# Kernel optimization log

Measured on AMD Instinct MI355X. Metric: run time of the kernel, lower is better.

The kernel has to match this reference:

```python
import jax, jax.numpy as jnp
import numpy as np

N, D, R, T, E = 4096, 1024, 92, 32, 8192
SCALE = float(np.sqrt(2.0 / 7.0))  # matches torch.rand(...) * sqrt(2/7)


def setup_inputs() -> dict:
    key = jax.random.key(0)
    ks = jax.random.split(key, 7)
    x = jax.random.normal(ks[0], (N, D), dtype=jnp.float32)
    edge_tok = jax.random.randint(ks[1], (E,), 0, N)
    edge_rel = jax.random.randint(ks[2], (E,), 0, R)
    W_stack = jax.random.uniform(ks[3], (R, D, D), dtype=jnp.float32) * SCALE  # depWeights
    B_stack = jnp.ones((R, D), dtype=jnp.float32)                              # depBias
    W_self = jax.random.uniform(ks[4], (D, D), dtype=jnp.float32) * SCALE      # self.weight
    b_self = jnp.ones((D,), dtype=jnp.float32)                                 # self.bias
    W_tag = jax.random.normal(ks[5], (D, T), dtype=jnp.float32) * 0.02         # hidden2tag
    b_tag = jnp.zeros((T,), dtype=jnp.float32)
    return {"x": x, "W_self": W_self, "b_self": b_self, "W_stack": W_stack,
            "B_stack": B_stack, "W_tag": W_tag, "b_tag": b_tag,
            "edge_tok": edge_tok, "edge_rel": edge_rel}


def reference(x, W_self, b_self, W_stack, B_stack, W_tag, b_tag, edge_tok, edge_rel):
    n, r = x.shape[0], W_stack.shape[0]
    # C[i, r] = number of dependency edges of token i with relation r
    C = jnp.zeros((n, r), dtype=x.dtype).at[edge_tok, edge_rel].add(jnp.asarray(1.0, x.dtype))
    self_out = x @ W_self + b_self  # [N, D]
    # accum_i = self_out_i + sum_{dep in deps(i)} (x_i @ W_dep + b_dep)
    #         = self_out_i + sum_r C[i, r] * (x_i @ W_r) + (C @ B_stack)_i
    def body(acc, wc):
        Wr, Cr = wc  # Wr: [D, D], Cr: [N]
        return acc + Cr[:, None] * (x @ Wr), None
    dep_out, _ = jax.lax.scan(body, jnp.zeros_like(self_out), (W_stack, C.T))
    h = jax.nn.relu(self_out + dep_out + C @ B_stack)  # [N, D]
    tag_scores = jax.nn.log_softmax(h @ W_tag + b_tag, axis=1)  # [N, T]
    return tag_scores, h
```

## Files before the change

kernel.cpp:

```cpp
#include <hip/hip_runtime.h>
#include <hip/hip_bf16.h>
#include <math.h>

#define N_TOK 4096
#define D_DIM 1024
#define R_REL 92
#define T_TAG 32
#define E_EDGE 8192
#define SELF_R 127
#define GRID_ITEMS 192


typedef short bf16x8 __attribute__((ext_vector_type(8)));
typedef float f32x4 __attribute__((ext_vector_type(4)));

union Pk8 { uint4 q; unsigned short s[8]; };
union Pk4 { uint2 d; unsigned short s[4]; };

__device__ __forceinline__ unsigned short f2bf(float f) {
    union { __hip_bfloat16 b; unsigned short u; } c;
    c.b = __float2bfloat16(f);
    return c.u;
}
__device__ __forceinline__ float bf2f(unsigned short u) {
    return __uint_as_float(((unsigned)u) << 16);
}
__device__ __forceinline__ void gload_lds16(const void* g, void* l) {
    __builtin_amdgcn_global_load_lds(
        (const __attribute__((address_space(1))) unsigned int*)g,
        (__attribute__((address_space(3))) unsigned int*)l, 16, 0, 0);
}

__global__ __launch_bounds__(1024) void k_prep(const int* __restrict__ rel,
                                               const int* __restrict__ tokv,
                                               const float* __restrict__ x,
                                               int* __restrict__ ws,
                                               unsigned short* __restrict__ xb) {
    int t = threadIdx.x;
    if (blockIdx.x > 0) {
        size_t base = ((size_t)(blockIdx.x - 1) * 1024 + t) * 8;
        float4 v0 = *(const float4*)(x + base);
        float4 v1 = *(const float4*)(x + base + 4);
        Pk8 u;
        u.s[0] = f2bf(v0.x); u.s[1] = f2bf(v0.y);
        u.s[2] = f2bf(v0.z); u.s[3] = f2bf(v0.w);
        u.s[4] = f2bf(v1.x); u.s[5] = f2bf(v1.y);
        u.s[6] = f2bf(v1.z); u.s[7] = f2bf(v1.w);
        *(uint4*)(xb + base) = u.q;
        return;
    }
    __shared__ int cnt[128], offL[128], cur[128];
    __shared__ int sh[128];
    __shared__ int wsum[16];
    __shared__ int tcnt[4096], toff[4096];
    int lane = t & 63, wid = t >> 6;
    if (t < 128) { cnt[t] = 0; cur[t] = 0; }
    #pragma unroll
    for (int i = 0; i < 4; ++i) tcnt[i * 1024 + t] = 0;
    __syncthreads();
    int er[8], et[8];
    #pragma unroll
    for (int i = 0; i < 8; ++i) {
        er[i] = rel[i * 1024 + t];
        et[i] = tokv[i * 1024 + t];
        atomicAdd(&cnt[er[i]], 1);
        atomicAdd(&tcnt[et[i]], 1);
    }
    __syncthreads();
    int c = (t < 128) ? cnt[t] : 0;
    int v = c;
    if (t < 128) sh[t] = v;
    __syncthreads();
    for (int st = 1; st < 128; st <<= 1) {
        int add = (t >= st && t < 128) ? sh[t - st] : 0;
        __syncthreads();
        if (t < 128) { v += add; sh[t] = v; }
        __syncthreads();
    }
    if (t < 128) { offL[t] = v - c; ws[256 + t] = v - c; ws[t] = c; }
    int ch = (t < R_REL) ? ((c + 127) >> 7) : 0;
    int v2 = ch;
    if (t < 128) sh[t] = v2;
    __syncthreads();
    for (int st = 1; st < 128; st <<= 1) {
        int add = (t >= st && t < 128) ? sh[t - st] : 0;
        __syncthreads();
        if (t < 128) { v2 += add; sh[t] = v2; }
        __syncthreads();
    }
    if (t < 32) ws[512 + t] = (SELF_R << 16) | t;
    if (t < R_REL) {
        int excl = v2 - ch;
        for (int j = 0; j < ch; ++j)
            ws[512 + 32 + excl + j] = (t << 16) | j;
    }
    if (t == 127) ws[384] = 32 + v2;
    int s0 = tcnt[4 * t + 0], s1 = tcnt[4 * t + 1];
    int s2 = tcnt[4 * t + 2], s3 = tcnt[4 * t + 3];
    int sum4 = s0 + s1 + s2 + s3;
    int vv = sum4;
    #pragma unroll
    for (int d = 1; d < 64; d <<= 1) {
        int n = __shfl_up(vv, d);
        if (lane >= d) vv += n;
    }
    if (lane == 63) wsum[wid] = vv;
    __syncthreads();
    if (wid == 0) {
        int wv = (lane < 16) ? wsum[lane] : 0;
        #pragma unroll
        for (int d = 1; d < 16; d <<= 1) {
            int n = __shfl_up(wv, d);
            if (lane >= d) wv += n;
        }
        if (lane < 16) wsum[lane] = wv;
    }
    __syncthreads();
    int base = (wid > 0) ? wsum[wid - 1] : 0;
    int incl = base + vv;
    int ex = incl - sum4;
    toff[4 * t + 0] = ex;
    toff[4 * t + 1] = ex + s0;
    toff[4 * t + 2] = ex + s0 + s1;
    toff[4 * t + 3] = ex + s0 + s1 + s2;
    ws[17408 + 4 * t + 0] = ex;
    ws[17408 + 4 * t + 1] = ex + s0;
    ws[17408 + 4 * t + 2] = ex + s0 + s1;
    ws[17408 + 4 * t + 3] = ex + s0 + s1 + s2;
    if (t == 1023) ws[17408 + 4096] = incl;
    __syncthreads();
    #pragma unroll
    for (int i = 0; i < 4; ++i) tcnt[i * 1024 + t] = 0;
    __syncthreads();
    #pragma unroll
    for (int i = 0; i < 8; ++i) {
        int pos = offL[er[i]] + atomicAdd(&cur[er[i]], 1);
        ws[1024 + pos] = et[i];
        int q = toff[et[i]] + atomicAdd(&tcnt[et[i]], 1);
        ws[22528 + q] = pos;
    }
}

__global__ __launch_bounds__(512, 4) void k_fused(const float* __restrict__ Wself,
                                                  const float* __restrict__ bself,
                                                  const float* __restrict__ Wst,
                                                  const float* __restrict__ Bst,
                                                  const int* __restrict__ ws,
                                                  const unsigned short* __restrict__ xb,
                                                  unsigned short* __restrict__ scratch) {
    if ((int)blockIdx.x >= ws[384]) return;
    int item = ws[512 + blockIdx.x];
    int r = item >> 16, chunk = item & 0xFFFF;
    int m0 = chunk * 128;
    int valid;
    const float* Wbase;
    const float* bias;
    bool is_self = (r == SELF_R);
    int off0 = 0;
    if (is_self) {
        valid = 128;
        Wbase = Wself;
        bias = bself;
    } else {
        int cnt = ws[r];
        off0 = ws[256 + r];
        valid = cnt - m0; if (valid > 128) valid = 128;
        Wbase = Wst + (size_t)r * D_DIM * D_DIM;
        bias = Bst + (size_t)r * D_DIM;
    }
    int srow_base = is_self ? (8192 + m0) : (off0 + m0);

    __shared__ unsigned short Al[2][8192];
    __shared__ unsigned short Bl[2][8192];
    __shared__ int toks[128];
    int t = threadIdx.x;
    if (t < 128) {
        int tok;
        if (is_self) tok = m0 + t;
        else tok = (t < valid) ? ws[1024 + off0 + m0 + t] : 0;
        toks[t] = tok;
    }
    __syncthreads();

    int gn0 = blockIdx.y * 128;
    int wid = t >> 6, l = t & 63;
    int lr = l & 15, lg = l >> 4;
    int wm = (wid >> 2) * 64, wn = (wid & 3) * 32;

    int row0 = wid * 16 + (l >> 3);
    int row1 = row0 + 8;
    const char* ga0 = (const char*)(xb + (size_t)toks[row0] * D_DIM) +
                      (((l & 7) * 16) ^ ((row0 & 7) << 4));
    const char* ga1 = (const char*)(xb + (size_t)toks[row1] * D_DIM) +
                      (((l & 7) * 16) ^ ((row1 & 7) << 4));

    int bcol = t & 127, bkq = t >> 7;
    const float* wp = Wbase + (size_t)bkq * 16 * D_DIM + gn0 + bcol;
    int bswz = (bcol & 7) << 4;
    int bb0 = bcol * 128 + ((bkq * 32) ^ bswz);
    int bb1 = bcol * 128 + ((bkq * 32 + 16) ^ bswz);

    float pb[16];
    gload_lds16(ga0, (char*)Al[0] + wid * 2048);
    gload_lds16(ga1, (char*)Al[0] + wid * 2048 + 1024);
    ga0 += 128; ga1 += 128;
    #pragma unroll
    for (int i = 0; i < 16; ++i) pb[i] = wp[(size_t)i * D_DIM];
    {
        Pk8 u0, u1;
        #pragma unroll
        for (int i = 0; i < 8; ++i) { u0.s[i] = f2bf(pb[i]); u1.s[i] = f2bf(pb[8 + i]); }
        *(uint4*)((char*)Bl[0] + bb0) = u0.q;
        *(uint4*)((char*)Bl[0] + bb1) = u1.q;
    }
    __syncthreads();

    f32x4 acc[4][2] = {};
    int cur = 0;
    for (int k0 = 0; k0 < D_DIM; k0 += 64) {
        bool pf = (k0 + 64 < D_DIM);
        int nxt = cur ^ 1;
        if (pf) {
            gload_lds16(ga0, (char*)Al[nxt] + wid * 2048);
            gload_lds16(ga1, (char*)Al[nxt] + wid * 2048 + 1024);
            ga0 += 128; ga1 += 128;
            #pragma unroll
            for (int i = 0; i < 16; ++i)
                pb[i] = wp[(size_t)(k0 + 64 + i) * D_DIM];
        }
        const char* Ac = (const char*)Al[cur];
        const char* Bc = (const char*)Bl[cur];
        #pragma unroll
        for (int kk = 0; kk < 2; ++kk) {
            int koff = kk * 64 + lg * 16;
            int sw = (lr & 7) << 4;
            bf16x8 af[4], bfr[2];
            #pragma unroll
            for (int mi = 0; mi < 4; ++mi)
                af[mi] = *(const bf16x8*)(Ac + (wm + mi * 16 + lr) * 128 + (koff ^ sw));
            #pragma unroll
            for (int ni = 0; ni < 2; ++ni)
                bfr[ni] = *(const bf16x8*)(Bc + (wn + ni * 16 + lr) * 128 + (koff ^ sw));
            #pragma unroll
            for (int mi = 0; mi < 4; ++mi)
                #pragma unroll
                for (int ni = 0; ni < 2; ++ni)
                    acc[mi][ni] = __builtin_amdgcn_mfma_f32_16x16x32_bf16(
                        af[mi], bfr[ni], acc[mi][ni], 0, 0, 0);
        }
        if (pf) {
            Pk8 u0, u1;
            #pragma unroll
            for (int i = 0; i < 8; ++i) { u0.s[i] = f2bf(pb[i]); u1.s[i] = f2bf(pb[8 + i]); }
            *(uint4*)((char*)Bl[nxt] + bb0) = u0.q;
            *(uint4*)((char*)Bl[nxt] + bb1) = u1.q;
        }
        __syncthreads();
        cur = nxt;
    }
    float bb[2];
    bb[0] = bias[gn0 + wn + lr];
    bb[1] = bias[gn0 + wn + 16 + lr];
    #pragma unroll
    for (int mi = 0; mi < 4; ++mi)
        #pragma unroll
        for (int j = 0; j < 4; ++j) {
            int rl = wm + mi * 16 + lg * 4 + j;
            if (rl < valid) {
                unsigned short* dst = scratch +
                    (size_t)(srow_base + rl) * D_DIM + gn0 + wn + lr;
                dst[0]  = f2bf(acc[mi][0][j] + bb[0]);
                dst[16] = f2bf(acc[mi][1][j] + bb[1]);
            }
        }
}

__global__ __launch_bounds__(256) void k_reduce(const int* __restrict__ ws,
                                                const unsigned short* __restrict__ scratch,
                                                float* __restrict__ out_h) {
    int tok = blockIdx.x;
    int t = threadIdx.x;
    int j0 = ws[17408 + tok], j1 = ws[17408 + tok + 1];
    ushort4 sv = *(const ushort4*)(scratch + (size_t)(8192 + tok) * D_DIM + t * 4);
    float a0 = bf2f(sv.x), a1 = bf2f(sv.y), a2 = bf2f(sv.z), a3 = bf2f(sv.w);
    for (int j = j0; j < j1; ++j) {
        int p = ws[22528 + j];
        ushort4 dv = *(const ushort4*)(scratch + (size_t)p * D_DIM + t * 4);
        a0 += bf2f(dv.x); a1 += bf2f(dv.y); a2 += bf2f(dv.z); a3 += bf2f(dv.w);
    }
    float4 o;
    o.x = fmaxf(a0, 0.f); o.y = fmaxf(a1, 0.f);
    o.z = fmaxf(a2, 0.f); o.w = fmaxf(a3, 0.f);
    *(float4*)(out_h + (size_t)tok * D_DIM + t * 4) = o;
}

__global__ __launch_bounds__(256) void k_tag(const float* __restrict__ out_h,
                                             const float* __restrict__ Wt,
                                             const float* __restrict__ bt,
                                             float* __restrict__ out_tag) {
    __shared__ unsigned short Al[64 * 64];
    __shared__ unsigned short Bl[32 * 64];
    char* Alb = (char*)Al;
    char* Blb = (char*)Bl;
    int tok0 = blockIdx.x * 64;
    int t = threadIdx.x;
    int w = t >> 6, l = t & 63, lr = l & 15, lg = l >> 4;
    int wm = w * 16;
    int ar = t >> 4, ac = t & 15;
    int bn = t & 31, kh = t >> 5;
    f32x4 acc[2] = {};
    for (int k0 = 0; k0 < D_DIM; k0 += 64) {
        __syncthreads();
        #pragma unroll
        for (int s = 0; s < 4; ++s) {
            int row = s * 16 + ar;
            const float* hp = out_h + (size_t)(tok0 + row) * D_DIM + k0 + ac * 4;
            float4 v = *(const float4*)hp;
            Pk4 u;
            u.s[0] = f2bf(v.x); u.s[1] = f2bf(v.y);
            u.s[2] = f2bf(v.z); u.s[3] = f2bf(v.w);
            *(uint2*)(Alb + row * 128 + ((ac * 8) ^ ((row & 7) << 4))) = u.d;
        }
        {
            Pk8 u;
            #pragma unroll
            for (int i = 0; i < 8; ++i)
                u.s[i] = f2bf(Wt[(size_t)(k0 + kh * 8 + i) * T_TAG + bn]);
            *(uint4*)(Blb + bn * 128 + ((kh * 16) ^ ((bn & 7) << 4))) = u.q;
        }
        __syncthreads();
        #pragma unroll
        for (int kk = 0; kk < 2; ++kk) {
            int koff = kk * 64 + lg * 16;
            bf16x8 af = *(const bf16x8*)(Alb + (wm + lr) * 128 +
                                         (koff ^ ((lr & 7) << 4)));
            #pragma unroll
            for (int ni = 0; ni < 2; ++ni) {
                bf16x8 bfr = *(const bf16x8*)(Blb + (ni * 16 + lr) * 128 +
                                              (koff ^ ((lr & 7) << 4)));
                acc[ni] = __builtin_amdgcn_mfma_f32_16x16x32_bf16(
                    af, bfr, acc[ni], 0, 0, 0);
            }
        }
    }
    float bt0 = bt[lr], bt1 = bt[16 + lr];
    #pragma unroll
    for (int j = 0; j < 4; ++j) {
        float v0 = acc[0][j] + bt0;
        float v1 = acc[1][j] + bt1;
        float m = fmaxf(v0, v1);
        #pragma unroll
        for (int s = 1; s < 16; s <<= 1) m = fmaxf(m, __shfl_xor(m, s));
        float sum = expf(v0 - m) + expf(v1 - m);
        #pragma unroll
        for (int s = 1; s < 16; s <<= 1) sum += __shfl_xor(sum, s);
        float lse = m + logf(sum);
        int row = tok0 + wm + lg * 4 + j;
        out_tag[(size_t)row * T_TAG + lr] = v0 - lse;
        out_tag[(size_t)row * T_TAG + 16 + lr] = v1 - lse;
    }
}

extern "C" void kernel_launch(void* const* d_in, const int* in_sizes, int n_in,
                              void* d_out, int out_size, void* d_ws, size_t ws_size,
                              hipStream_t stream) {
    const float* x     = (const float*)d_in[0];
    const float* Wself = (const float*)d_in[1];
    const float* bself = (const float*)d_in[2];
    const float* Wst   = (const float*)d_in[3];
    const float* Bst   = (const float*)d_in[4];
    const float* Wtag  = (const float*)d_in[5];
    const float* btag  = (const float*)d_in[6];
    const int*   etok  = (const int*)d_in[7];
    const int*   erel  = (const int*)d_in[8];
    float* out_tag = (float*)d_out;
    float* out_h   = (float*)d_out + (size_t)N_TOK * T_TAG;
    int* ws = (int*)d_ws;
    unsigned short* scratch = (unsigned short*)((int*)d_ws + 32768);
    unsigned short* xb = scratch + (size_t)12288 * 1024;

    k_prep<<<513, 1024, 0, stream>>>(erel, etok, x, ws, xb);
    k_fused<<<dim3(GRID_ITEMS, D_DIM / 128), 512, 0, stream>>>(
        Wself, bself, Wst, Bst, ws, xb, scratch);
    k_reduce<<<N_TOK, 256, 0, stream>>>(ws, scratch, out_h);
    k_tag<<<N_TOK / 64, 256, 0, stream>>>(out_h, Wtag, btag, out_tag);
}
```

Measured before the change: 144.6 us.

## Deepen GEMM pipeline with two register B buffers and manual vmcnt waits

Restructures the gathered GEMM main loop into a manually unrolled ping-pong schedule. Two register buffers hold fp32 W tiles so that the global loads for tile k+2 are issued while tile k is consumed. Explicit s_waitcnt vmcnt counts, raw s_barrier and sched_barrier replace __syncthreads to keep loads in flight across the barrier. The aim is to hide global load latency more deeply, at the cost of more registers and fragile hand-counted wait values.

```diff
diff --git a/kernel.cpp b/kernel.cpp
--- a/kernel.cpp
+++ b/kernel.cpp
@@ -200,64 +200,76 @@
     int bb0 = bcol * 128 + ((bkq * 32) ^ bswz);
     int bb1 = bcol * 128 + ((bkq * 32 + 16) ^ bswz);
 
-    float pb[16];
-    gload_lds16(ga0, (char*)Al[0] + wid * 2048);
-    gload_lds16(ga1, (char*)Al[0] + wid * 2048 + 1024);
-    ga0 += 128; ga1 += 128;
-    #pragma unroll
-    for (int i = 0; i < 16; ++i) pb[i] = wp[(size_t)i * D_DIM];
-    {
-        Pk8 u0, u1;
-        #pragma unroll
-        for (int i = 0; i < 8; ++i) { u0.s[i] = f2bf(pb[i]); u1.s[i] = f2bf(pb[8 + i]); }
-        *(uint4*)((char*)Bl[0] + bb0) = u0.q;
-        *(uint4*)((char*)Bl[0] + bb1) = u1.q;
-    }
-    __syncthreads();
-
+    float pbA[16], pbB[16];
     f32x4 acc[4][2] = {};
-    int cur = 0;
-    for (int k0 = 0; k0 < D_DIM; k0 += 64) {
-        bool pf = (k0 + 64 < D_DIM);
-        int nxt = cur ^ 1;
-        if (pf) {
-            gload_lds16(ga0, (char*)Al[nxt] + wid * 2048);
-            gload_lds16(ga1, (char*)Al[nxt] + wid * 2048 + 1024);
-            ga0 += 128; ga1 += 128;
-            #pragma unroll
-            for (int i = 0; i < 16; ++i)
-                pb[i] = wp[(size_t)(k0 + 64 + i) * D_DIM];
-        }
-        const char* Ac = (const char*)Al[cur];
-        const char* Bc = (const char*)Bl[cur];
-        #pragma unroll
-        for (int kk = 0; kk < 2; ++kk) {
-            int koff = kk * 64 + lg * 16;
-            int sw = (lr & 7) << 4;
-            bf16x8 af[4], bfr[2];
-            #pragma unroll
-            for (int mi = 0; mi < 4; ++mi)
-                af[mi] = *(const bf16x8*)(Ac + (wm + mi * 16 + lr) * 128 + (koff ^ sw));
-            #pragma unroll
-            for (int ni = 0; ni < 2; ++ni)
-                bfr[ni] = *(const bf16x8*)(Bc + (wn + ni * 16 + lr) * 128 + (koff ^ sw));
-            #pragma unroll
-            for (int mi = 0; mi < 4; ++mi)
-                #pragma unroll
-                for (int ni = 0; ni < 2; ++ni)
-                    acc[mi][ni] = __builtin_amdgcn_mfma_f32_16x16x32_bf16(
-                        af[mi], bfr[ni], acc[mi][ni], 0, 0, 0);
-        }
-        if (pf) {
-            Pk8 u0, u1;
-            #pragma unroll
-            for (int i = 0; i < 8; ++i) { u0.s[i] = f2bf(pb[i]); u1.s[i] = f2bf(pb[8 + i]); }
-            *(uint4*)((char*)Bl[nxt] + bb0) = u0.q;
-            *(uint4*)((char*)Bl[nxt] + bb1) = u1.q;
-        }
-        __syncthreads();
-        cur = nxt;
-    }
+
+#define A_ISSUE(BUF) { gload_lds16(ga0, (char*)(BUF) + wid * 2048); \
+                       gload_lds16(ga1, (char*)(BUF) + wid * 2048 + 1024); \
+                       ga0 += 128; ga1 += 128; }
+#define B_ISSUE(PB) { _Pragma("unroll") \
+                      for (int i_ = 0; i_ < 16; ++i_) PB[i_] = wp[(size_t)i_ * D_DIM]; \
+                      wp += (size_t)64 * D_DIM; }
+#define B_CVT(PB, BUF) { Pk8 u0_, u1_; \
+                         _Pragma("unroll") \
+                         for (int i_ = 0; i_ < 8; ++i_) { u0_.s[i_] = f2bf(PB[i_]); u1_.s[i_] = f2bf(PB[8 + i_]); } \
+                         *(uint4*)((char*)(BUF) + bb0) = u0_.q; \
+                         *(uint4*)((char*)(BUF) + bb1) = u1_.q; }
+#define MFMA_PHASE(ABUF, BBUF) { const char* Ac_ = (const char*)(ABUF); \
+        const char* Bc_ = (const char*)(BBUF); \
+        _Pragma("unroll") \
+        for (int kk = 0; kk < 2; ++kk) { \
+            int koff = kk * 64 + lg * 16; \
+            int sw = (lr & 7) << 4; \
+            bf16x8 af[4], bfr[2]; \
+            _Pragma("unroll") \
+            for (int mi = 0; mi < 4; ++mi) \
+                af[mi] = *(const bf16x8*)(Ac_ + (wm + mi * 16 + lr) * 128 + (koff ^ sw)); \
+            _Pragma("unroll") \
+            for (int ni = 0; ni < 2; ++ni) \
+                bfr[ni] = *(const bf16x8*)(Bc_ + (wn + ni * 16 + lr) * 128 + (koff ^ sw)); \
+            _Pragma("unroll") \
+            for (int mi = 0; mi < 4; ++mi) \
+                _Pragma("unroll") \
+                for (int ni = 0; ni < 2; ++ni) \
+                    acc[mi][ni] = __builtin_amdgcn_mfma_f32_16x16x32_bf16( \
+                        af[mi], bfr[ni], acc[mi][ni], 0, 0, 0); } }
+#define KBAR(VM) { asm volatile("s_waitcnt vmcnt(" VM ") lgkmcnt(0)" ::: "memory"); \
+                   __builtin_amdgcn_s_barrier(); \
+                   __builtin_amdgcn_sched_barrier(0); }
+
+    A_ISSUE(Al[0]);
+    B_ISSUE(pbA);
+    B_ISSUE(pbB);
+    asm volatile("s_waitcnt vmcnt(16)" ::: "memory");
+    B_CVT(pbA, Bl[0]);
+    asm volatile("s_waitcnt lgkmcnt(0)" ::: "memory");
+    __builtin_amdgcn_s_barrier();
+    __builtin_amdgcn_sched_barrier(0);
+
+    for (int tp = 0; tp < 7; ++tp) {
+        A_ISSUE(Al[1]);
+        B_ISSUE(pbA);
+        MFMA_PHASE(Al[0], Bl[0]);
+        B_CVT(pbB, Bl[1]);
+        KBAR("16");
+        A_ISSUE(Al[0]);
+        B_ISSUE(pbB);
+        MFMA_PHASE(Al[1], Bl[1]);
+        B_CVT(pbA, Bl[0]);
+        KBAR("16");
+    }
+    A_ISSUE(Al[1]);
+    MFMA_PHASE(Al[0], Bl[0]);
+    B_CVT(pbB, Bl[1]);
+    KBAR("0");
+    MFMA_PHASE(Al[1], Bl[1]);
+
+#undef A_ISSUE
+#undef B_ISSUE
+#undef B_CVT
+#undef MFMA_PHASE
+#undef KBAR
+
     float bb[2];
     bb[0] = bias[gn0 + wn + lr];
     bb[1] = bias[gn0 + wn + 16 + lr];
```

Result: slower. 152.4 us (+5.4%).

## Fuse gather-reduce and tag projection into one kernel

Applied to the files above, without the earlier changes.

Merges the per-token gather/sum/ReLU kernel with the tag matmul + log_softmax kernel, so each 32-token block builds h on the fly, writes it out, and feeds the bf16 copy straight into LDS for the MFMA. This avoids re-reading h (16 MB fp32) from global memory and removes one launch. The cost is a much smaller grid (128 blocks of 128 threads), which lowers parallelism for the memory-bound gather phase, and a serial k-loop that interleaves gather latency with MFMA work.

```diff
diff --git a/kernel.cpp b/kernel.cpp
--- a/kernel.cpp
+++ b/kernel.cpp
@@ -275,69 +275,97 @@
         }
 }
 
-__global__ __launch_bounds__(256) void k_reduce(const int* __restrict__ ws,
+__global__ __launch_bounds__(128) void k_redtag(const int* __restrict__ ws,
                                                 const unsigned short* __restrict__ scratch,
-                                                float* __restrict__ out_h) {
-    int tok = blockIdx.x;
-    int t = threadIdx.x;
-    int j0 = ws[17408 + tok], j1 = ws[17408 + tok + 1];
-    ushort4 sv = *(const ushort4*)(scratch + (size_t)(8192 + tok) * D_DIM + t * 4);
-    float a0 = bf2f(sv.x), a1 = bf2f(sv.y), a2 = bf2f(sv.z), a3 = bf2f(sv.w);
-    for (int j = j0; j < j1; ++j) {
-        int p = ws[22528 + j];
-        ushort4 dv = *(const ushort4*)(scratch + (size_t)p * D_DIM + t * 4);
-        a0 += bf2f(dv.x); a1 += bf2f(dv.y); a2 += bf2f(dv.z); a3 += bf2f(dv.w);
-    }
-    float4 o;
-    o.x = fmaxf(a0, 0.f); o.y = fmaxf(a1, 0.f);
-    o.z = fmaxf(a2, 0.f); o.w = fmaxf(a3, 0.f);
-    *(float4*)(out_h + (size_t)tok * D_DIM + t * 4) = o;
-}
-
-__global__ __launch_bounds__(256) void k_tag(const float* __restrict__ out_h,
-                                             const float* __restrict__ Wt,
-                                             const float* __restrict__ bt,
-                                             float* __restrict__ out_tag) {
-    __shared__ unsigned short Al[64 * 64];
+                                                const float* __restrict__ Wt,
+                                                const float* __restrict__ bt,
+                                                float* __restrict__ out_h,
+                                                float* __restrict__ out_tag) {
+    __shared__ unsigned short Al[32 * 64];
     __shared__ unsigned short Bl[32 * 64];
+    __shared__ int j0s[32], j1s[32];
     char* Alb = (char*)Al;
     char* Blb = (char*)Bl;
-    int tok0 = blockIdx.x * 64;
+    int tok0 = blockIdx.x * 32;
     int t = threadIdx.x;
+    if (t < 32) {
+        j0s[t] = ws[17408 + tok0 + t];
+        j1s[t] = ws[17408 + tok0 + t + 1];
+    }
     int w = t >> 6, l = t & 63, lr = l & 15, lg = l >> 4;
     int wm = w * 16;
-    int ar = t >> 4, ac = t & 15;
-    int bn = t & 31, kh = t >> 5;
+    int row = t >> 2, c16 = (t & 3) * 16;
+    int bn = t & 31, kh = (t >> 5) & 3;
     f32x4 acc[2] = {};
     for (int k0 = 0; k0 < D_DIM; k0 += 64) {
         __syncthreads();
-        #pragma unroll
-        for (int s = 0; s < 4; ++s) {
-            int row = s * 16 + ar;
-            const float* hp = out_h + (size_t)(tok0 + row) * D_DIM + k0 + ac * 4;
-            float4 v = *(const float4*)hp;
-            Pk4 u;
-            u.s[0] = f2bf(v.x); u.s[1] = f2bf(v.y);
-            u.s[2] = f2bf(v.z); u.s[3] = f2bf(v.w);
-            *(uint2*)(Alb + row * 128 + ((ac * 8) ^ ((row & 7) << 4))) = u.d;
-        }
         {
+            int tok = tok0 + row;
+            const unsigned short* sp =
+                scratch + (size_t)(8192 + tok) * D_DIM + k0 + c16;
+            Pk8 v0, v1;
+            v0.q = *(const uint4*)sp;
+            v1.q = *(const uint4*)(sp + 8);
+            float a[16];
+            #pragma unroll
+            for (int i = 0; i < 8; ++i) {
+                a[i] = bf2f(v0.s[i]);
+                a[8 + i] = bf2f(v1.s[i]);
+            }
+            for (int j = j0s[row]; j < j1s[row]; ++j) {
+                int p = ws[22528 + j];
+                const unsigned short* dp =
+                    scratch + (size_t)p * D_DIM + k0 + c16;
+                Pk8 d0, d1;
+                d0.q = *(const uint4*)dp;
+                d1.q = *(const uint4*)(dp + 8);
+                #pragma unroll
+                for (int i = 0; i < 8; ++i) {
+                    a[i] += bf2f(d0.s[i]);
+                    a[8 + i] += bf2f(d1.s[i]);
+                }
+            }
+            #pragma unroll
+            for (int i = 0; i < 16; ++i) a[i] = fmaxf(a[i], 0.f);
+            float* hp = out_h + (size_t)tok * D_DIM + k0 + c16;
+            #pragma unroll
+            for (int q = 0; q < 4; ++q) {
+                float4 o;
+                o.x = a[4 * q]; o.y = a[4 * q + 1];
+                o.z = a[4 * q + 2]; o.w = a[4 * q + 3];
+                *(float4*)(hp + 4 * q) = o;
+            }
+            Pk8 u0, u1;
+            #pragma unroll
+            for (int i = 0; i < 8; ++i) {
+                u0.s[i] = f2bf(a[i]);
+                u1.s[i] = f2bf(a[8 + i]);
+            }
+            int sw = (row & 7) << 4;
+            *(uint4*)(Alb + row * 128 + ((c16 * 2) ^ sw)) = u0.q;
+            *(uint4*)(Alb + row * 128 + ((c16 * 2 + 16) ^ sw)) = u1.q;
+        }
+        {
+            int swb = (bn & 7) << 4;
             Pk8 u;
             #pragma unroll
             for (int i = 0; i < 8; ++i)
-                u.s[i] = f2bf(Wt[(size_t)(k0 + kh * 8 + i) * T_TAG + bn]);
-            *(uint4*)(Blb + bn * 128 + ((kh * 16) ^ ((bn & 7) << 4))) = u.q;
+                u.s[i] = f2bf(Wt[(size_t)(k0 + kh * 16 + i) * T_TAG + bn]);
+            *(uint4*)(Blb + bn * 128 + ((kh * 32) ^ swb)) = u.q;
+            #pragma unroll
+            for (int i = 0; i < 8; ++i)
+                u.s[i] = f2bf(Wt[(size_t)(k0 + kh * 16 + 8 + i) * T_TAG + bn]);
+            *(uint4*)(Blb + bn * 128 + ((kh * 32 + 16) ^ swb)) = u.q;
         }
         __syncthreads();
         #pragma unroll
         for (int kk = 0; kk < 2; ++kk) {
             int koff = kk * 64 + lg * 16;
-            bf16x8 af = *(const bf16x8*)(Alb + (wm + lr) * 128 +
-                                         (koff ^ ((lr & 7) << 4)));
+            int sw = (lr & 7) << 4;
+            bf16x8 af = *(const bf16x8*)(Alb + (wm + lr) * 128 + (koff ^ sw));
             #pragma unroll
             for (int ni = 0; ni < 2; ++ni) {
-                bf16x8 bfr = *(const bf16x8*)(Blb + (ni * 16 + lr) * 128 +
-                                              (koff ^ ((lr & 7) << 4)));
+                bf16x8 bfr = *(const bf16x8*)(Blb + (ni * 16 + lr) * 128 + (koff ^ sw));
                 acc[ni] = __builtin_amdgcn_mfma_f32_16x16x32_bf16(
                     af, bfr, acc[ni], 0, 0, 0);
             }
@@ -355,9 +383,9 @@
         #pragma unroll
         for (int s = 1; s < 16; s <<= 1) sum += __shfl_xor(sum, s);
         float lse = m + logf(sum);
-        int row = tok0 + wm + lg * 4 + j;
-        out_tag[(size_t)row * T_TAG + lr] = v0 - lse;
-        out_tag[(size_t)row * T_TAG + 16 + lr] = v1 - lse;
+        int rowo = tok0 + wm + lg * 4 + j;
+        out_tag[(size_t)rowo * T_TAG + lr] = v0 - lse;
+        out_tag[(size_t)rowo * T_TAG + 16 + lr] = v1 - lse;
     }
 }
 
@@ -382,6 +410,5 @@
     k_prep<<<513, 1024, 0, stream>>>(erel, etok, x, ws, xb);
     k_fused<<<dim3(GRID_ITEMS, D_DIM / 128), 512, 0, stream>>>(
         Wself, bself, Wst, Bst, ws, xb, scratch);
-    k_reduce<<<N_TOK, 256, 0, stream>>>(ws, scratch, out_h);
-    k_tag<<<N_TOK / 64, 256, 0, stream>>>(out_h, Wtag, btag, out_tag);
-}
+    k_redtag<<<N_TOK / 32, 128, 0, stream>>>(ws, scratch, Wtag, btag, out_h, out_tag);
+}
```

New measurement: 189.9 us. +31.4%, slower.

## Split tag GEMM K dimension across waves with LDS reduction, more blocks

Applied to the files above, without the earlier changes.

The tag projection kernel now processes 16 tokens per block instead of 64, launching 256 blocks instead of 64. Each of the four waves handles its own quarter of the K dimension in private LDS buffers with no per-step block barriers, then partials are summed through shared memory before log-softmax. The aim is better GPU occupancy and fewer syncs in a small kernel, at the cost of reloading W_tag four times as often and a final cross-wave reduction.

```diff
diff --git a/kernel.cpp b/kernel.cpp
--- a/kernel.cpp
+++ b/kernel.cpp
@@ -298,66 +298,78 @@
                                              const float* __restrict__ Wt,
                                              const float* __restrict__ bt,
                                              float* __restrict__ out_tag) {
-    __shared__ unsigned short Al[64 * 64];
-    __shared__ unsigned short Bl[32 * 64];
-    char* Alb = (char*)Al;
-    char* Blb = (char*)Bl;
-    int tok0 = blockIdx.x * 64;
+    __shared__ unsigned short Abuf[4][16 * 64];
+    __shared__ unsigned short Bbuf[4][32 * 64];
+    __shared__ float red[4][2][256];
+    int tok0 = blockIdx.x * 16;
     int t = threadIdx.x;
     int w = t >> 6, l = t & 63, lr = l & 15, lg = l >> 4;
-    int wm = w * 16;
-    int ar = t >> 4, ac = t & 15;
-    int bn = t & 31, kh = t >> 5;
+    char* Ab = (char*)Abuf[w];
+    char* Bb = (char*)Bbuf[w];
+    int kbase = w * 256;
+    int arow = l >> 2, ak = (l & 3) * 16;
+    int btag = l >> 1, bk = (l & 1) * 32;
     f32x4 acc[2] = {};
-    for (int k0 = 0; k0 < D_DIM; k0 += 64) {
-        __syncthreads();
-        #pragma unroll
-        for (int s = 0; s < 4; ++s) {
-            int row = s * 16 + ar;
-            const float* hp = out_h + (size_t)(tok0 + row) * D_DIM + k0 + ac * 4;
-            float4 v = *(const float4*)hp;
-            Pk4 u;
-            u.s[0] = f2bf(v.x); u.s[1] = f2bf(v.y);
-            u.s[2] = f2bf(v.z); u.s[3] = f2bf(v.w);
-            *(uint2*)(Alb + row * 128 + ((ac * 8) ^ ((row & 7) << 4))) = u.d;
-        }
+    for (int kc = 0; kc < 4; ++kc) {
+        int k0 = kbase + kc * 64;
         {
-            Pk8 u;
-            #pragma unroll
-            for (int i = 0; i < 8; ++i)
-                u.s[i] = f2bf(Wt[(size_t)(k0 + kh * 8 + i) * T_TAG + bn]);
-            *(uint4*)(Blb + bn * 128 + ((kh * 16) ^ ((bn & 7) << 4))) = u.q;
-        }
-        __syncthreads();
+            const float* hp = out_h + (size_t)(tok0 + arow) * D_DIM + k0 + ak;
+            Pk8 u0, u1;
+            #pragma unroll
+            for (int i = 0; i < 8; ++i) { u0.s[i] = f2bf(hp[i]); u1.s[i] = f2bf(hp[8 + i]); }
+            int sw = (arow & 7) << 4;
+            *(uint4*)(Ab + arow * 128 + ((ak * 2) ^ sw)) = u0.q;
+            *(uint4*)(Ab + arow * 128 + ((ak * 2 + 16) ^ sw)) = u1.q;
+        }
+        {
+            int sw = (btag & 7) << 4;
+            #pragma unroll
+            for (int q = 0; q < 4; ++q) {
+                Pk8 u;
+                #pragma unroll
+                for (int i = 0; i < 8; ++i)
+                    u.s[i] = f2bf(Wt[(size_t)(k0 + bk + q * 8 + i) * T_TAG + btag]);
+                *(uint4*)(Bb + btag * 128 + ((bk * 2 + q * 16) ^ sw)) = u.q;
+            }
+        }
         #pragma unroll
         for (int kk = 0; kk < 2; ++kk) {
             int koff = kk * 64 + lg * 16;
-            bf16x8 af = *(const bf16x8*)(Alb + (wm + lr) * 128 +
-                                         (koff ^ ((lr & 7) << 4)));
+            int sw = (lr & 7) << 4;
+            bf16x8 af = *(const bf16x8*)(Ab + lr * 128 + (koff ^ sw));
             #pragma unroll
             for (int ni = 0; ni < 2; ++ni) {
-                bf16x8 bfr = *(const bf16x8*)(Blb + (ni * 16 + lr) * 128 +
-                                              (koff ^ ((lr & 7) << 4)));
+                bf16x8 bfr = *(const bf16x8*)(Bb + (ni * 16 + lr) * 128 + (koff ^ sw));
                 acc[ni] = __builtin_amdgcn_mfma_f32_16x16x32_bf16(
                     af, bfr, acc[ni], 0, 0, 0);
             }
         }
     }
-    float bt0 = bt[lr], bt1 = bt[16 + lr];
-    #pragma unroll
-    for (int j = 0; j < 4; ++j) {
-        float v0 = acc[0][j] + bt0;
-        float v1 = acc[1][j] + bt1;
-        float m = fmaxf(v0, v1);
-        #pragma unroll
-        for (int s = 1; s < 16; s <<= 1) m = fmaxf(m, __shfl_xor(m, s));
-        float sum = expf(v0 - m) + expf(v1 - m);
-        #pragma unroll
-        for (int s = 1; s < 16; s <<= 1) sum += __shfl_xor(sum, s);
-        float lse = m + logf(sum);
-        int row = tok0 + wm + lg * 4 + j;
-        out_tag[(size_t)row * T_TAG + lr] = v0 - lse;
-        out_tag[(size_t)row * T_TAG + 16 + lr] = v1 - lse;
+    #pragma unroll
+    for (int ni = 0; ni < 2; ++ni)
+        #pragma unroll
+        for (int j = 0; j < 4; ++j)
+            red[w][ni][j * 64 + l] = acc[ni][j];
+    __syncthreads();
+    if (w == 0) {
+        float bt0 = bt[lr], bt1 = bt[16 + lr];
+        #pragma unroll
+        for (int j = 0; j < 4; ++j) {
+            float v0 = red[0][0][j * 64 + l] + red[1][0][j * 64 + l] +
+                       red[2][0][j * 64 + l] + red[3][0][j * 64 + l] + bt0;
+            float v1 = red[0][1][j * 64 + l] + red[1][1][j * 64 + l] +
+                       red[2][1][j * 64 + l] + red[3][1][j * 64 + l] + bt1;
+            float m = fmaxf(v0, v1);
+            #pragma unroll
+            for (int s = 1; s < 16; s <<= 1) m = fmaxf(m, __shfl_xor(m, s));
+            float sum = expf(v0 - m) + expf(v1 - m);
+            #pragma unroll
+            for (int s = 1; s < 16; s <<= 1) sum += __shfl_xor(sum, s);
+            float lse = m + logf(sum);
+            int row = tok0 + lg * 4 + j;
+            out_tag[(size_t)row * T_TAG + lr] = v0 - lse;
+            out_tag[(size_t)row * T_TAG + 16 + lr] = v1 - lse;
+        }
     }
 }
 
@@ -383,5 +395,5 @@
     k_fused<<<dim3(GRID_ITEMS, D_DIM / 128), 512, 0, stream>>>(
         Wself, bself, Wst, Bst, ws, xb, scratch);
     k_reduce<<<N_TOK, 256, 0, stream>>>(ws, scratch, out_h);
-    k_tag<<<N_TOK / 64, 256, 0, stream>>>(out_h, Wtag, btag, out_tag);
-}
+    k_tag<<<N_TOK / 16, 256, 0, stream>>>(out_h, Wtag, btag, out_tag);
+}
```

Result: slower. 147.9 us (median of 2 runs) (+2.3%).
